# Optimization experiments

Hardware: AMD Instinct MI355X
Metric: run time of the kernel (lower is better)

The kernel has to match this reference:

```python
import jax, jax.numpy as jnp
import numpy as np

NEG_INF = -1.0e12  # matches masked_fill value in the torch module


def _entmax15(x, axis=-1):
    """Exact entmax with alpha=1.5 (Peters & Martins, 2019), sort-based."""
    x = x - jnp.max(x, axis=axis, keepdims=True)
    x = x / 2.0
    d = x.shape[axis]
    xs = -jnp.sort(-x, axis=axis)  # descending sort along normalization axis
    rho = jnp.arange(1, d + 1, dtype=x.dtype)  # 1..d, broadcasts on last axis
    mean = jnp.cumsum(xs, axis=axis) / rho
    mean_sq = jnp.cumsum(xs * xs, axis=axis) / rho
    ss = rho * (mean_sq - mean * mean)
    delta = (1.0 - ss) / rho
    tau = mean - jnp.sqrt(jnp.clip(delta, 0.0))
    support = jnp.sum((tau <= xs).astype(jnp.int32), axis=axis, keepdims=True)
    tau_star = jnp.take_along_axis(tau, support - 1, axis=axis)
    y = jnp.clip(x - tau_star, 0.0)
    return y * y


def setup_inputs() -> dict:
    key = jax.random.key(0)
    kq, kk, kv, km = jax.random.split(key, 4)
    B, H, S, D = 4, 8, 1024, 128
    q = jax.random.normal(kq, (B, H, S, D), dtype=jnp.float32)
    k = jax.random.normal(kk, (B, H, S, D), dtype=jnp.float32)
    v = jax.random.normal(kv, (B, H, S, D), dtype=jnp.float32)
    mask = jax.random.randint(km, (B, 1, S, S), 0, 2, dtype=jnp.int32)
    return {"q": q, "k": k, "v": v, "mask": mask}


def reference(q, k, v, mask):
    D = q.shape[-1]
    scale = 1.0 / jnp.sqrt(jnp.asarray(D, dtype=q.dtype))
    scores = jnp.einsum("bhqd,bhkd->bhqk", q, k) * scale
    scores = jnp.where(mask == 0, jnp.asarray(NEG_INF, dtype=scores.dtype), scores)
    attn = _entmax15(scores, axis=-1)
    return jnp.einsum("bhqk,bhkd->bhqd", attn, v)
```

## Files before the change

### kernel.cpp

```cpp
#include <hip/hip_runtime.h>


#define S_ 1024
#define D_ 128
#define NEG_INF_F (-1.0e12f)
#define SCALE_F 0.08838834764831845f
#define NITER 14
#define SCP 1028
#define CCAP 512
#define CSTR 516

typedef float f32x4 __attribute__((ext_vector_type(4)));
typedef short short8 __attribute__((ext_vector_type(8)));

__device__ __forceinline__ ushort f2bf(float x) {
    unsigned u = __builtin_bit_cast(unsigned, x);
    u += 0x7FFFu + ((u >> 16) & 1u);
    return (ushort)(u >> 16);
}
__device__ __forceinline__ float bf2f(ushort h) {
    unsigned u = ((unsigned)h) << 16;
    return __builtin_bit_cast(float, u);
}

__global__ __launch_bounds__(256)
void pre_cvt(const float* __restrict__ K, const float* __restrict__ V,
             ushort* __restrict__ Kb, ushort* __restrict__ Vt)
{
    __shared__ ushort tile[64][72];
    const int t = threadIdx.x;
    if (blockIdx.x < 4096) {
        int i = blockIdx.x * 256 + t;
        float4 v = ((const float4*)K)[i];
        ushort4 o;
        o.x = f2bf(v.x); o.y = f2bf(v.y); o.z = f2bf(v.z); o.w = f2bf(v.w);
        ((ushort4*)Kb)[i] = o;
        return;
    }
    const int vb = blockIdx.x - 4096;
    const int bh = vb >> 5, r5 = vb & 31, kt = r5 >> 1, dh = r5 & 1;
    const float* src = V + ((size_t)(bh * S_ + kt * 64)) * D_ + dh * 64;
    #pragma unroll
    for (int i = 0; i < 4; ++i) {
        int idx = t + i * 256, r = idx >> 4, c = idx & 15;
        float4 vv = *(const float4*)(src + (size_t)r * D_ + c * 4);
        ushort4 o;
        o.x = f2bf(vv.x); o.y = f2bf(vv.y); o.z = f2bf(vv.z); o.w = f2bf(vv.w);
        *(ushort4*)&tile[r][c * 4] = o;
    }
    __syncthreads();
    ushort* dst = Vt + ((size_t)(bh * D_ + dh * 64)) * S_ + kt * 64;
    #pragma unroll
    for (int i = 0; i < 2; ++i) {
        int idx = t + i * 256, d = idx >> 3, jj = idx & 7;
        short8 val; ushort* vp = (ushort*)&val;
        #pragma unroll
        for (int e = 0; e < 8; ++e) vp[e] = tile[jj * 8 + e][d];
        *(short8*)(dst + (size_t)d * S_ + jj * 8) = val;
    }
}

__global__ __launch_bounds__(512, 4)
void entmax_attn(const float* __restrict__ Q, const ushort* __restrict__ Kb,
                 const ushort* __restrict__ Vt, const int* __restrict__ M,
                 float* __restrict__ O)
{
    __shared__ __align__(16) ushort sc[16][SCP];
    __shared__ __align__(16) ushort kv[128][136];
    __shared__ __align__(16) ushort q_s[16][136];

    const int t = threadIdx.x;
    const int w = t >> 6, lane = t & 63, l = lane & 15, quad = lane >> 4;
    const int bh = blockIdx.x >> 6, qt = blockIdx.x & 63, b = bh >> 3;

    const ushort* kb_bh = Kb + (size_t)bh * S_ * D_;
    const ushort* vt_bh = Vt + (size_t)bh * D_ * S_;

    int cr[4], cc[4];
    #pragma unroll
    for (int i = 0; i < 4; ++i) {
        int cell = t + i * 512;
        cr[i] = cell >> 4; cc[i] = cell & 15;
    }

    {
        const float4* qsrc = (const float4*)(Q + ((size_t)bh * S_ + (size_t)qt * 16) * D_);
        int r = t >> 5, c = t & 31;
        float4 v = qsrc[r * 32 + c];
        ushort4 o;
        o.x = f2bf(v.x); o.y = f2bf(v.y); o.z = f2bf(v.z); o.w = f2bf(v.w);
        *(ushort4*)&q_s[r][c * 4] = o;
    }
    short8 sreg[4];
    #pragma unroll
    for (int i = 0; i < 4; ++i)
        sreg[i] = *(const short8*)(kb_bh + (size_t)cr[i] * D_ + cc[i] * 8);

    __syncthreads();

    short8 aq[4];
    #pragma unroll
    for (int ks = 0; ks < 4; ++ks)
        aq[ks] = *(const short8*)&q_s[l][ks * 32 + quad * 8];

    #pragma unroll
    for (int i = 0; i < 4; ++i) *(short8*)&kv[cr[i]][cc[i] * 8] = sreg[i];
    __syncthreads();

    #pragma unroll 1
    for (int kt = 0; kt < 8; ++kt) {
        if (kt < 7) {
            const ushort* nb = kb_bh + (size_t)(kt + 1) * 128 * D_;
            #pragma unroll
            for (int i = 0; i < 4; ++i)
                sreg[i] = *(const short8*)(nb + (size_t)cr[i] * D_ + cc[i] * 8);
        }
        f32x4 acc = {0.f, 0.f, 0.f, 0.f};
        const int n = w * 16 + l;
        #pragma unroll
        for (int ks = 0; ks < 4; ++ks) {
            short8 bk = *(const short8*)&kv[n][ks * 32 + quad * 8];
            acc = __builtin_amdgcn_mfma_f32_16x16x32_bf16(aq[ks], bk, acc, 0, 0, 0);
        }
        #pragma unroll
        for (int r = 0; r < 4; ++r)
            sc[quad * 4 + r][kt * 128 + w * 16 + l] = f2bf(acc[r] * SCALE_F);
        __syncthreads();
        if (kt < 7) {
            #pragma unroll
            for (int i = 0; i < 4; ++i) *(short8*)&kv[cr[i]][cc[i] * 8] = sreg[i];
            __syncthreads();
        }
    }

    #pragma unroll
    for (int i = 0; i < 4; ++i)
        sreg[i] = *(const short8*)(vt_bh + (size_t)cr[i] * S_ + cc[i] * 8);

    const int row = t >> 5, u = t & 31;
    const int qg = qt * 16 + row;
    float x[32];
    #pragma unroll
    for (int c = 0; c < 4; ++c) {
        short8 v8 = *(const short8*)&sc[row][c * 256 + u * 8];
        #pragma unroll
        for (int e = 0; e < 8; ++e) x[c * 8 + e] = bf2f(((ushort*)&v8)[e]);
    }
    {
        const int4* mrow = (const int4*)(M + ((size_t)b * S_ + qg) * S_);
        #pragma unroll
        for (int c = 0; c < 4; ++c) {
            #pragma unroll
            for (int h = 0; h < 2; ++h) {
                int4 mm = mrow[c * 64 + u * 2 + h];
                if (mm.x == 0) x[c * 8 + h * 4 + 0] = NEG_INF_F;
                if (mm.y == 0) x[c * 8 + h * 4 + 1] = NEG_INF_F;
                if (mm.z == 0) x[c * 8 + h * 4 + 2] = NEG_INF_F;
                if (mm.w == 0) x[c * 8 + h * 4 + 3] = NEG_INF_F;
            }
        }
    }
    float mx = -3.0e38f;
    #pragma unroll
    for (int j = 0; j < 32; ++j) mx = fmaxf(mx, x[j]);
    #pragma unroll
    for (int off = 1; off < 32; off <<= 1) mx = fmaxf(mx, __shfl_xor(mx, off));
    #pragma unroll
    for (int j = 0; j < 32; ++j) x[j] = (x[j] - mx) * 0.5f;

    float* cand = (float*)&kv[0][0];
    const unsigned long long halfmask =
        (lane >= 32) ? 0xFFFFFFFF00000000ull : 0x00000000FFFFFFFFull;
    int cnt = 0;
    #pragma unroll
    for (int j = 0; j < 32; ++j) {
        const bool p = (x[j] > -1.0f);
        unsigned long long bal = __ballot(p) & halfmask;
        if (p) {
            int pos = cnt + (int)__builtin_amdgcn_mbcnt_hi(
                (unsigned)(bal >> 32),
                __builtin_amdgcn_mbcnt_lo((unsigned)bal, 0));
            if (pos < CCAP) cand[row * CSTR + pos] = x[j];
        }
        cnt += __popcll(bal);
    }

    float tau;
    if (cnt <= CCAP) {
        const float* crow = cand + row * CSTR;
        float lo = -1.f, hi = 0.f;
        #pragma unroll 1
        for (int it = 0; it < NITER; ++it) {
            const float tm = 0.5f * (lo + hi);
            float f = 0.f;
            for (int j = u; j < cnt; j += 32) {
                float d = fmaxf(crow[j] - tm, 0.f);
                f = fmaf(d, d, f);
            }
            #pragma unroll
            for (int off = 1; off < 32; off <<= 1) f += __shfl_xor(f, off);
            const bool ge = (f >= 1.f);
            lo = ge ? tm : lo;
            hi = ge ? hi : tm;
        }
        tau = 0.5f * (lo + hi);
    } else {
        float lo = -1.f, hi = 0.f;
        #pragma unroll 1
        for (int it = 0; it < NITER; ++it) {
            const float tm = 0.5f * (lo + hi);
            float f = 0.f;
            #pragma unroll
            for (int j = 0; j < 32; ++j) {
                float d = fmaxf(x[j] - tm, 0.f);
                f = fmaf(d, d, f);
            }
            #pragma unroll
            for (int off = 1; off < 32; off <<= 1) f += __shfl_xor(f, off);
            const bool ge = (f >= 1.f);
            lo = ge ? tm : lo;
            hi = ge ? hi : tm;
        }
        tau = 0.5f * (lo + hi);
    }

    #pragma unroll
    for (int c = 0; c < 4; ++c) {
        short8 v8;
        #pragma unroll
        for (int e = 0; e < 8; ++e) {
            float d = fmaxf(x[c * 8 + e] - tau, 0.f);
            ((ushort*)&v8)[e] = f2bf(d * d);
        }
        *(short8*)&sc[row][c * 256 + u * 8] = v8;
    }
    __syncthreads();
    #pragma unroll
    for (int i = 0; i < 4; ++i) *(short8*)&kv[cr[i]][cc[i] * 8] = sreg[i];
    __syncthreads();

    f32x4 oa = {0.f, 0.f, 0.f, 0.f};
    #pragma unroll 1
    for (int vt = 0; vt < 8; ++vt) {
        if (vt < 7) {
            const ushort* nb = vt_bh + (size_t)(vt + 1) * 128;
            #pragma unroll
            for (int i = 0; i < 4; ++i)
                sreg[i] = *(const short8*)(nb + (size_t)cr[i] * S_ + cc[i] * 8);
        }
        const int d = w * 16 + l;
        #pragma unroll
        for (int ki = 0; ki < 4; ++ki) {
            short8 ap = *(const short8*)&sc[l][vt * 128 + ki * 32 + quad * 8];
            short8 bv = *(const short8*)&kv[d][ki * 32 + quad * 8];
            oa = __builtin_amdgcn_mfma_f32_16x16x32_bf16(ap, bv, oa, 0, 0, 0);
        }
        __syncthreads();
        if (vt < 7) {
            #pragma unroll
            for (int i = 0; i < 4; ++i) *(short8*)&kv[cr[i]][cc[i] * 8] = sreg[i];
            __syncthreads();
        }
    }

    float* ob = O + ((size_t)bh * S_ + (size_t)qt * 16) * D_;
    #pragma unroll
    for (int r = 0; r < 4; ++r)
        ob[(size_t)(quad * 4 + r) * D_ + w * 16 + l] = oa[r];
}

extern "C" void kernel_launch(void* const* d_in, const int* in_sizes, int n_in,
                              void* d_out, int out_size, void* d_ws, size_t ws_size,
                              hipStream_t stream) {
    const float* q = (const float*)d_in[0];
    const float* k = (const float*)d_in[1];
    const float* v = (const float*)d_in[2];
    const int*   m = (const int*)d_in[3];
    float*       o = (float*)d_out;

    ushort* Kb = (ushort*)d_ws;
    ushort* Vt = (ushort*)((char*)d_ws + 8388608);

    pre_cvt<<<5120, 256, 0, stream>>>(k, v, Kb, Vt);
    entmax_attn<<<2048, 512, 0, stream>>>(q, Kb, Vt, m, o);
}
```

Before: 206.0 us.

## Shrink LDS with XOR-swizzled half-width K/V tiles to raise occupancy

Drops the padded shared-memory layouts and uses XOR swizzling to avoid bank conflicts. The K/V staging tile is halved to 64 columns, so the QK and PV loops now run 16 half-steps instead of 8, and the candidate buffer capacity is cut to 256. This shrinks LDS so launch bounds can request 6 blocks per CU, and the MFMA sections are wrapped in s_setprio. The pre-conversion kernel now writes V transposed into shared memory so it can read rows with vector loads. The cost is twice as many barriers, and rows with more than 256 candidates fall back to the slower path more often.

```diff
diff --git a/kernel.cpp b/kernel.cpp
--- a/kernel.cpp
+++ b/kernel.cpp
@@ -6,9 +6,7 @@
 #define NEG_INF_F (-1.0e12f)
 #define SCALE_F 0.08838834764831845f
 #define NITER 14
-#define SCP 1028
-#define CCAP 512
-#define CSTR 516
+#define CCAP 256
 
 typedef float f32x4 __attribute__((ext_vector_type(4)));
 typedef short short8 __attribute__((ext_vector_type(8)));
@@ -27,7 +25,7 @@
 void pre_cvt(const float* __restrict__ K, const float* __restrict__ V,
              ushort* __restrict__ Kb, ushort* __restrict__ Vt)
 {
-    __shared__ ushort tile[64][72];
+    __shared__ __align__(16) ushort tileT[64][68];
     const int t = threadIdx.x;
     if (blockIdx.x < 4096) {
         int i = blockIdx.x * 256 + t;
@@ -44,30 +42,29 @@
     for (int i = 0; i < 4; ++i) {
         int idx = t + i * 256, r = idx >> 4, c = idx & 15;
         float4 vv = *(const float4*)(src + (size_t)r * D_ + c * 4);
-        ushort4 o;
-        o.x = f2bf(vv.x); o.y = f2bf(vv.y); o.z = f2bf(vv.z); o.w = f2bf(vv.w);
-        *(ushort4*)&tile[r][c * 4] = o;
+        tileT[c * 4 + 0][r] = f2bf(vv.x);
+        tileT[c * 4 + 1][r] = f2bf(vv.y);
+        tileT[c * 4 + 2][r] = f2bf(vv.z);
+        tileT[c * 4 + 3][r] = f2bf(vv.w);
     }
     __syncthreads();
     ushort* dst = Vt + ((size_t)(bh * D_ + dh * 64)) * S_ + kt * 64;
     #pragma unroll
     for (int i = 0; i < 2; ++i) {
         int idx = t + i * 256, d = idx >> 3, jj = idx & 7;
-        short8 val; ushort* vp = (ushort*)&val;
-        #pragma unroll
-        for (int e = 0; e < 8; ++e) vp[e] = tile[jj * 8 + e][d];
+        short8 val = *(const short8*)&tileT[d][jj * 8];
         *(short8*)(dst + (size_t)d * S_ + jj * 8) = val;
     }
 }
 
-__global__ __launch_bounds__(512, 4)
+__global__ __launch_bounds__(512, 6)
 void entmax_attn(const float* __restrict__ Q, const ushort* __restrict__ Kb,
                  const ushort* __restrict__ Vt, const int* __restrict__ M,
                  float* __restrict__ O)
 {
-    __shared__ __align__(16) ushort sc[16][SCP];
-    __shared__ __align__(16) ushort kv[128][136];
-    __shared__ __align__(16) ushort q_s[16][136];
+    __shared__ __align__(16) ushort sc[16][1024];
+    __shared__ __align__(16) ushort kv[128][64];
+    __shared__ __align__(16) ushort q_s[16][128];
 
     const int t = threadIdx.x;
     const int w = t >> 6, lane = t & 63, l = lane & 15, quad = lane >> 4;
@@ -76,12 +73,9 @@
     const ushort* kb_bh = Kb + (size_t)bh * S_ * D_;
     const ushort* vt_bh = Vt + (size_t)bh * D_ * S_;
 
-    int cr[4], cc[4];
-    #pragma unroll
-    for (int i = 0; i < 4; ++i) {
-        int cell = t + i * 512;
-        cr[i] = cell >> 4; cc[i] = cell & 15;
-    }
+    const int sr0 = t >> 3, sch = t & 7, sr1 = sr0 + 64;
+    ushort* kvw0 = &kv[sr0][(sch ^ (sr0 & 7)) << 3];
+    ushort* kvw1 = &kv[sr1][(sch ^ (sr0 & 7)) << 3];
 
     {
         const float4* qsrc = (const float4*)(Q + ((size_t)bh * S_ + (size_t)qt * 16) * D_);
@@ -89,60 +83,69 @@
         float4 v = qsrc[r * 32 + c];
         ushort4 o;
         o.x = f2bf(v.x); o.y = f2bf(v.y); o.z = f2bf(v.z); o.w = f2bf(v.w);
-        *(ushort4*)&q_s[r][c * 4] = o;
-    }
-    short8 sreg[4];
-    #pragma unroll
-    for (int i = 0; i < 4; ++i)
-        sreg[i] = *(const short8*)(kb_bh + (size_t)cr[i] * D_ + cc[i] * 8);
-
+        *(ushort4*)&q_s[r][(((c >> 1) ^ (r & 7)) << 3) + ((c & 1) << 2)] = o;
+    }
+    short8 s0 = *(const short8*)(kb_bh + (size_t)sr0 * D_ + sch * 8);
+    short8 s1 = *(const short8*)(kb_bh + (size_t)sr1 * D_ + sch * 8);
+    *(short8*)kvw0 = s0;
+    *(short8*)kvw1 = s1;
     __syncthreads();
 
     short8 aq[4];
     #pragma unroll
     for (int ks = 0; ks < 4; ++ks)
-        aq[ks] = *(const short8*)&q_s[l][ks * 32 + quad * 8];
-
-    #pragma unroll
-    for (int i = 0; i < 4; ++i) *(short8*)&kv[cr[i]][cc[i] * 8] = sreg[i];
-    __syncthreads();
+        aq[ks] = *(const short8*)&q_s[l][((ks * 4 + quad) ^ (l & 7)) << 3];
+
+    const int n = w * 16 + l;
+    const ushort* kvA = &kv[n][(quad ^ (l & 7)) << 3];
+    const ushort* kvB = &kv[n][((4 + quad) ^ (l & 7)) << 3];
 
     #pragma unroll 1
     for (int kt = 0; kt < 8; ++kt) {
-        if (kt < 7) {
-            const ushort* nb = kb_bh + (size_t)(kt + 1) * 128 * D_;
-            #pragma unroll
-            for (int i = 0; i < 4; ++i)
-                sreg[i] = *(const short8*)(nb + (size_t)cr[i] * D_ + cc[i] * 8);
-        }
         f32x4 acc = {0.f, 0.f, 0.f, 0.f};
-        const int n = w * 16 + l;
-        #pragma unroll
-        for (int ks = 0; ks < 4; ++ks) {
-            short8 bk = *(const short8*)&kv[n][ks * 32 + quad * 8];
-            acc = __builtin_amdgcn_mfma_f32_16x16x32_bf16(aq[ks], bk, acc, 0, 0, 0);
-        }
-        #pragma unroll
-        for (int r = 0; r < 4; ++r)
-            sc[quad * 4 + r][kt * 128 + w * 16 + l] = f2bf(acc[r] * SCALE_F);
-        __syncthreads();
-        if (kt < 7) {
-            #pragma unroll
-            for (int i = 0; i < 4; ++i) *(short8*)&kv[cr[i]][cc[i] * 8] = sreg[i];
+        #pragma unroll
+        for (int kh = 0; kh < 2; ++kh) {
+            const int h = kt * 2 + kh;
+            if (h < 15) {
+                const int h2 = h + 1;
+                const ushort* nb = kb_bh + (size_t)(h2 >> 1) * (128 * D_) + (h2 & 1) * 64;
+                s0 = *(const short8*)(nb + (size_t)sr0 * D_ + sch * 8);
+                s1 = *(const short8*)(nb + (size_t)sr1 * D_ + sch * 8);
+            }
+            __builtin_amdgcn_s_setprio(1);
+            {
+                short8 bk0 = *(const short8*)kvA;
+                short8 bk1 = *(const short8*)kvB;
+                acc = __builtin_amdgcn_mfma_f32_16x16x32_bf16(aq[kh * 2 + 0], bk0, acc, 0, 0, 0);
+                acc = __builtin_amdgcn_mfma_f32_16x16x32_bf16(aq[kh * 2 + 1], bk1, acc, 0, 0, 0);
+            }
+            __builtin_amdgcn_s_setprio(0);
+            if (kh == 1) {
+                #pragma unroll
+                for (int r = 0; r < 4; ++r) {
+                    const int rr = quad * 4 + r, col = kt * 128 + n;
+                    sc[rr][(((col >> 3) ^ (rr & 7)) << 3) + (col & 7)] =
+                        f2bf(acc[r] * SCALE_F);
+                }
+            }
             __syncthreads();
-        }
-    }
-
-    #pragma unroll
-    for (int i = 0; i < 4; ++i)
-        sreg[i] = *(const short8*)(vt_bh + (size_t)cr[i] * S_ + cc[i] * 8);
+            if (h < 15) {
+                *(short8*)kvw0 = s0;
+                *(short8*)kvw1 = s1;
+                __syncthreads();
+            }
+        }
+    }
+
+    s0 = *(const short8*)(vt_bh + (size_t)sr0 * S_ + sch * 8);
+    s1 = *(const short8*)(vt_bh + (size_t)sr1 * S_ + sch * 8);
 
     const int row = t >> 5, u = t & 31;
     const int qg = qt * 16 + row;
     float x[32];
     #pragma unroll
     for (int c = 0; c < 4; ++c) {
-        short8 v8 = *(const short8*)&sc[row][c * 256 + u * 8];
+        short8 v8 = *(const short8*)&sc[row][((c * 32 + u) ^ (row & 7)) << 3];
         #pragma unroll
         for (int e = 0; e < 8; ++e) x[c * 8 + e] = bf2f(((ushort*)&v8)[e]);
     }
@@ -180,14 +183,14 @@
             int pos = cnt + (int)__builtin_amdgcn_mbcnt_hi(
                 (unsigned)(bal >> 32),
                 __builtin_amdgcn_mbcnt_lo((unsigned)bal, 0));
-            if (pos < CCAP) cand[row * CSTR + pos] = x[j];
+            if (pos < CCAP) cand[row * CCAP + pos] = x[j];
         }
         cnt += __popcll(bal);
     }
 
     float tau;
     if (cnt <= CCAP) {
-        const float* crow = cand + row * CSTR;
+        const float* crow = cand + row * CCAP;
         float lo = -1.f, hi = 0.f;
         #pragma unroll 1
         for (int it = 0; it < NITER; ++it) {
@@ -232,33 +235,35 @@
             float d = fmaxf(x[c * 8 + e] - tau, 0.f);
             ((ushort*)&v8)[e] = f2bf(d * d);
         }
-        *(short8*)&sc[row][c * 256 + u * 8] = v8;
-    }
-    __syncthreads();
-    #pragma unroll
-    for (int i = 0; i < 4; ++i) *(short8*)&kv[cr[i]][cc[i] * 8] = sreg[i];
+        *(short8*)&sc[row][((c * 32 + u) ^ (row & 7)) << 3] = v8;
+    }
+    __syncthreads();
+    *(short8*)kvw0 = s0;
+    *(short8*)kvw1 = s1;
     __syncthreads();
 
     f32x4 oa = {0.f, 0.f, 0.f, 0.f};
     #pragma unroll 1
-    for (int vt = 0; vt < 8; ++vt) {
-        if (vt < 7) {
-            const ushort* nb = vt_bh + (size_t)(vt + 1) * 128;
-            #pragma unroll
-            for (int i = 0; i < 4; ++i)
-                sreg[i] = *(const short8*)(nb + (size_t)cr[i] * S_ + cc[i] * 8);
-        }
-        const int d = w * 16 + l;
-        #pragma unroll
-        for (int ki = 0; ki < 4; ++ki) {
-            short8 ap = *(const short8*)&sc[l][vt * 128 + ki * 32 + quad * 8];
-            short8 bv = *(const short8*)&kv[d][ki * 32 + quad * 8];
-            oa = __builtin_amdgcn_mfma_f32_16x16x32_bf16(ap, bv, oa, 0, 0, 0);
-        }
+    for (int vh = 0; vh < 16; ++vh) {
+        if (vh < 15) {
+            const ushort* nb = vt_bh + (size_t)(vh + 1) * 64;
+            s0 = *(const short8*)(nb + (size_t)sr0 * S_ + sch * 8);
+            s1 = *(const short8*)(nb + (size_t)sr1 * S_ + sch * 8);
+        }
+        __builtin_amdgcn_s_setprio(1);
+        {
+            short8 ap0 = *(const short8*)&sc[l][((vh * 8 + quad) ^ (l & 7)) << 3];
+            short8 ap1 = *(const short8*)&sc[l][((vh * 8 + 4 + quad) ^ (l & 7)) << 3];
+            short8 bv0 = *(const short8*)kvA;
+            short8 bv1 = *(const short8*)kvB;
+            oa = __builtin_amdgcn_mfma_f32_16x16x32_bf16(ap0, bv0, oa, 0, 0, 0);
+            oa = __builtin_amdgcn_mfma_f32_16x16x32_bf16(ap1, bv1, oa, 0, 0, 0);
+        }
+        __builtin_amdgcn_s_setprio(0);
         __syncthreads();
-        if (vt < 7) {
-            #pragma unroll
-            for (int i = 0; i < 4; ++i) *(short8*)&kv[cr[i]][cc[i] * 8] = sreg[i];
+        if (vh < 15) {
+            *(short8*)kvw0 = s0;
+            *(short8*)kvw1 = s1;
             __syncthreads();
         }
     }
```

Result: faster. 190.4 us (-7.6%).
